# Performance work log

Measured on AMD Instinct MI355X. Metric: run time of the kernel, lower is better.

The kernel has to match this reference:

```python
import jax, jax.numpy as jnp
import numpy as np

N, D = 1024, 64
C = 1.0
MIN_NORM = 1e-15
PROJ_EPS = 4e-3  # HGCN float32 boundary eps


def _artanh(z):
    return jnp.arctanh(jnp.clip(z, -1.0 + 1e-7, 1.0 - 1e-7))


def _mobius_add(x, y, c):
    x2 = jnp.sum(x * x, -1, keepdims=True)
    y2 = jnp.sum(y * y, -1, keepdims=True)
    xy = jnp.sum(x * y, -1, keepdims=True)
    num = (1.0 + 2.0 * c * xy + c * y2) * x + (1.0 - c * x2) * y
    den = 1.0 + 2.0 * c * xy + c * c * x2 * y2
    return num / jnp.maximum(den, MIN_NORM)


def _lambda_x(p, c):
    return 2.0 / jnp.maximum(1.0 - c * jnp.sum(p * p, -1, keepdims=True), MIN_NORM)


def _logmap0(p, c):
    sqrt_c = c ** 0.5
    pn = jnp.maximum(jnp.linalg.norm(p, axis=-1, keepdims=True), MIN_NORM)
    return _artanh(sqrt_c * pn) * p / (sqrt_c * pn)


def _logmap(p1, p2, c):
    # tangent at p1 pointing toward p2 (broadcasts)
    sub = _mobius_add(-p1, p2, c)
    sn = jnp.maximum(jnp.linalg.norm(sub, axis=-1, keepdims=True), MIN_NORM)
    lam = _lambda_x(p1, c)
    sqrt_c = c ** 0.5
    return (2.0 / (sqrt_c * lam)) * _artanh(sqrt_c * sn) * sub / sn


def _expmap(u, p, c):
    # exp at p of tangent u (HGCN signature expmap(u, p, c))
    sqrt_c = c ** 0.5
    un = jnp.maximum(jnp.linalg.norm(u, axis=-1, keepdims=True), MIN_NORM)
    second = jnp.tanh(sqrt_c * _lambda_x(p, c) * un / 2.0) * u / (sqrt_c * un)
    return _mobius_add(p, second, c)


def _proj(x, c):
    sqrt_c = c ** 0.5
    n = jnp.maximum(jnp.linalg.norm(x, axis=-1, keepdims=True), MIN_NORM)
    maxnorm = (1.0 - PROJ_EPS) / sqrt_c
    return jnp.where(n > maxnorm, x / n * maxnorm, x)


def setup_inputs() -> dict:
    key = jax.random.key(0)
    k1, k2, k3 = jax.random.split(key, 3)
    x = 0.1 * jax.random.normal(k1, (N, D), jnp.float32)
    x = _proj(x, C)  # points on the Poincare ball
    adj = (jax.random.uniform(k2, (N, N)) < 0.02).astype(jnp.float32)
    att_W = jax.random.normal(k3, (2 * D, 1), jnp.float32) / np.sqrt(2 * D).astype(np.float32)
    att_b = jnp.zeros((1,), jnp.float32)
    return {"x": x, "adj": adj, "att_W": att_W, "att_b": att_b}


def reference(x, adj, att_W, att_b):
    # x_tangent = logmap0(x)
    x_tan = _logmap0(x, C)
    # DenseAtt: sigmoid(Linear(cat(x_i, x_j))) * adj, without materializing [N,N,2D]
    left = x_tan @ att_W[:D] + att_b   # [N,1]
    right = x_tan @ att_W[D:]          # [N,1]
    adj_att = jax.nn.sigmoid(left + right.T) * adj  # [N,N]
    # local tangent vectors: logmap at x_i of every x_j -> [N,N,D]
    x_local = _logmap(x[:, None, :], x[None, :, :], C)
    support_t = jnp.einsum('ij,ijd->id', adj_att, x_local)  # [N,D]
    return _proj(_expmap(x, support_t, C), C)
```

## Files before the change

kernel.cpp:

```cpp
#include <hip/hip_runtime.h>
#include <math.h>

#define NN 1024
#define DD 64
#define MIN_NORM 1e-15f
#define ART_BOUND (1.0f - 1e-7f)

__device__ __forceinline__ float wave_sum(float v) {
#pragma unroll
    for (int off = 32; off >= 1; off >>= 1)
        v += __shfl_xor(v, off, 64);
    return v;
}

__device__ __forceinline__ float artanh_f(float z) {
    z = fminf(z, ART_BOUND);
    return 0.5f * __logf((1.0f + z) / (1.0f - z));
}

__global__ __launch_bounds__(64) void hypagg_pre_kernel(
    const float* __restrict__ x, const float* __restrict__ W,
    const float* __restrict__ b, float* __restrict__ x2_out,
    float* __restrict__ left_out, float* __restrict__ right_out) {
    const int i = blockIdx.x;
    const int d = threadIdx.x;
    const float xd = x[i * DD + d];
    const float x2 = wave_sum(xd * xd);
    const float pn = fmaxf(sqrtf(x2), MIN_NORM);
    const float xt = artanh_f(pn) * xd / pn;
    const float l = wave_sum(xt * W[d]);
    const float r = wave_sum(xt * W[DD + d]);
    if (d == 0) {
        x2_out[i] = x2;
        left_out[i] = l + b[0];
        right_out[i] = r;
    }
}

__global__ __launch_bounds__(256) void hypagg_main_kernel(
    const float* __restrict__ x, const float* __restrict__ adj,
    const float* __restrict__ x2v, const float* __restrict__ leftv,
    const float* __restrict__ rightv, float* __restrict__ out) {
    __shared__ float sSd[4][DD];
    __shared__ float sAl[4];

    const int i = blockIdx.x;
    const int tid = threadIdx.x;
    const int w = tid >> 6;
    const int lane = tid & 63;

    const float xi = x[i * DD + lane];
    const float x2i = x2v[i];
    const float li = leftv[i];
    const float Bc = 1.0f - x2i;
    const float fac_i = fmaxf(Bc, MIN_NORM);

    float av[4];
#pragma unroll
    for (int kk = 0; kk < 4; ++kk)
        av[kk] = adj[i * NN + (4 * w + kk) * 64 + lane];

    float Sd = 0.0f;
    float alpha = 0.0f;

#pragma unroll
    for (int kk = 0; kk < 4; ++kk) {
        unsigned long long mask = __ballot(av[kk] != 0.0f);
        while (mask) {
            const int bit = __builtin_ctzll(mask);
            mask &= mask - 1;
            const int j = (4 * w + kk) * 64 + bit;
            const float adjv = __shfl(av[kk], bit, 64);
            const float xj = x[j * DD + lane];
            const float y2 = x2v[j];
            const float rj = rightv[j];
            const float dot = wave_sum(xi * xj);
            const float wgt = adjv / (1.0f + __expf(-(li + rj)));
            const float A = 1.0f - 2.0f * dot + y2;
            const float den = fmaxf(1.0f - 2.0f * dot + x2i * y2, MIN_NORM);
            const float sn2 = (A * A * x2i - 2.0f * A * Bc * dot + Bc * Bc * y2) / (den * den);
            const float sn = sqrtf(fmaxf(sn2, 0.0f));
            const float snc = fmaxf(sn, MIN_NORM);
            const float g = wgt * fac_i * artanh_f(sn) / (snc * den);
            Sd += g * xj;
            alpha -= g * A;
        }
    }

    sSd[w][lane] = Sd;
    if (lane == 0) sAl[w] = alpha;
    __syncthreads();

    if (w == 0) {
        const float S = sSd[0][lane] + sSd[1][lane] + sSd[2][lane] + sSd[3][lane];
        const float al = sAl[0] + sAl[1] + sAl[2] + sAl[3];
        const float accd = al * xi + Bc * S;

        const float p2 = wave_sum(accd * accd);
        const float un = fmaxf(sqrtf(x2i), MIN_NORM);
        const float lam_p = 2.0f / fmaxf(1.0f - p2, MIN_NORM);
        const float tt = tanhf(lam_p * un * 0.5f);
        const float second = tt * xi / un;
        const float y2e = wave_sum(second * second);
        const float xye = wave_sum(accd * second);
        const float Ae = 1.0f + 2.0f * xye + y2e;
        const float dene = fmaxf(1.0f + 2.0f * xye + p2 * y2e, MIN_NORM);
        const float res = (Ae * accd + (1.0f - p2) * second) / dene;
        const float n2 = wave_sum(res * res);
        const float n = fmaxf(sqrtf(n2), MIN_NORM);
        const float maxnorm = 1.0f - 4e-3f;
        const float o = (n > maxnorm) ? res * (maxnorm / n) : res;
        out[i * DD + lane] = o;
    }
}

extern "C" void kernel_launch(void* const* d_in, const int* in_sizes, int n_in,
                              void* d_out, int out_size, void* d_ws, size_t ws_size,
                              hipStream_t stream) {
    const float* x   = (const float*)d_in[0];
    const float* adj = (const float*)d_in[1];
    const float* W   = (const float*)d_in[2];
    const float* b   = (const float*)d_in[3];
    float* out = (float*)d_out;

    float* x2v    = (float*)d_ws;
    float* leftv  = x2v + NN;
    float* rightv = leftv + NN;

    hipLaunchKernelGGL(hypagg_pre_kernel, dim3(NN), dim3(DD), 0, stream,
                       x, W, b, x2v, leftv, rightv);
    hipLaunchKernelGGL(hypagg_main_kernel, dim3(NN), dim3(256), 0, stream,
                       x, adj, x2v, leftv, rightv, out);
}
```

Before: 73.94 us.

## Compact neighbor lists in LDS and process neighbor pairs with interleaved reductions

Each wave now compacts its nonzero adjacency entries into a shared-memory list using ballot and mbcnt prefix counts. It then processes neighbors two at a time, so two independent gathers and two shuffle reductions are interleaved and latency can overlap. The pre-kernel packs four rows per 256-thread block to cut block count. The cost is extra LDS, more registers and a tail loop for odd counts.

```diff
diff --git a/kernel.cpp b/kernel.cpp
--- a/kernel.cpp
+++ b/kernel.cpp
@@ -18,12 +18,12 @@
     return 0.5f * __logf((1.0f + z) / (1.0f - z));
 }
 
-__global__ __launch_bounds__(64) void hypagg_pre_kernel(
+__global__ __launch_bounds__(256) void hypagg_pre_kernel(
     const float* __restrict__ x, const float* __restrict__ W,
     const float* __restrict__ b, float* __restrict__ x2_out,
     float* __restrict__ left_out, float* __restrict__ right_out) {
-    const int i = blockIdx.x;
-    const int d = threadIdx.x;
+    const int i = blockIdx.x * 4 + (threadIdx.x >> 6);
+    const int d = threadIdx.x & 63;
     const float xd = x[i * DD + d];
     const float x2 = wave_sum(xd * xd);
     const float pn = fmaxf(sqrtf(x2), MIN_NORM);
@@ -41,6 +41,8 @@
     const float* __restrict__ x, const float* __restrict__ adj,
     const float* __restrict__ x2v, const float* __restrict__ leftv,
     const float* __restrict__ rightv, float* __restrict__ out) {
+    __shared__ int   sjL[4][256];
+    __shared__ float saL[4][256];
     __shared__ float sSd[4][DD];
     __shared__ float sAl[4];
 
@@ -52,29 +54,53 @@
     const float xi = x[i * DD + lane];
     const float x2i = x2v[i];
     const float li = leftv[i];
-    const float Bc = 1.0f - x2i;
-    const float fac_i = fmaxf(Bc, MIN_NORM);
-
     float av[4];
 #pragma unroll
     for (int kk = 0; kk < 4; ++kk)
         av[kk] = adj[i * NN + (4 * w + kk) * 64 + lane];
 
+    const float Bc = 1.0f - x2i;
+    const float fac_i = fmaxf(Bc, MIN_NORM);
+
+    int base = 0;
+#pragma unroll
+    for (int kk = 0; kk < 4; ++kk) {
+        const unsigned long long m = __ballot(av[kk] != 0.0f);
+        if (av[kk] != 0.0f) {
+            const int pos = __builtin_amdgcn_mbcnt_hi(
+                (unsigned int)(m >> 32),
+                __builtin_amdgcn_mbcnt_lo((unsigned int)m, 0u));
+            sjL[w][base + pos] = (4 * w + kk) * 64 + lane;
+            saL[w][base + pos] = av[kk];
+        }
+        base += __popcll(m);
+    }
+    const int M = base;
+
     float Sd = 0.0f;
     float alpha = 0.0f;
 
+    int t = 0;
+    for (; t + 2 <= M; t += 2) {
+        const int ja = sjL[w][t], jb = sjL[w][t + 1];
+        const float aa = saL[w][t], ab = saL[w][t + 1];
+        const float xa = x[ja * DD + lane];
+        const float xb = x[jb * DD + lane];
+        const float y2a = x2v[ja], y2b = x2v[jb];
+        const float rja = rightv[ja], rjb = rightv[jb];
+        float da = xi * xa, db = xi * xb;
 #pragma unroll
-    for (int kk = 0; kk < 4; ++kk) {
-        unsigned long long mask = __ballot(av[kk] != 0.0f);
-        while (mask) {
-            const int bit = __builtin_ctzll(mask);
-            mask &= mask - 1;
-            const int j = (4 * w + kk) * 64 + bit;
-            const float adjv = __shfl(av[kk], bit, 64);
-            const float xj = x[j * DD + lane];
-            const float y2 = x2v[j];
-            const float rj = rightv[j];
-            const float dot = wave_sum(xi * xj);
+        for (int off = 32; off >= 1; off >>= 1) {
+            da += __shfl_xor(da, off, 64);
+            db += __shfl_xor(db, off, 64);
+        }
+#pragma unroll
+        for (int q = 0; q < 2; ++q) {
+            const float dot = (q == 0) ? da : db;
+            const float y2 = (q == 0) ? y2a : y2b;
+            const float rj = (q == 0) ? rja : rjb;
+            const float adjv = (q == 0) ? aa : ab;
+            const float xq = (q == 0) ? xa : xb;
             const float wgt = adjv / (1.0f + __expf(-(li + rj)));
             const float A = 1.0f - 2.0f * dot + y2;
             const float den = fmaxf(1.0f - 2.0f * dot + x2i * y2, MIN_NORM);
@@ -82,9 +108,26 @@
             const float sn = sqrtf(fmaxf(sn2, 0.0f));
             const float snc = fmaxf(sn, MIN_NORM);
             const float g = wgt * fac_i * artanh_f(sn) / (snc * den);
-            Sd += g * xj;
+            Sd += g * xq;
             alpha -= g * A;
         }
+    }
+    for (; t < M; ++t) {
+        const int j = sjL[w][t];
+        const float adjv = saL[w][t];
+        const float xj = x[j * DD + lane];
+        const float y2 = x2v[j];
+        const float rj = rightv[j];
+        const float dot = wave_sum(xi * xj);
+        const float wgt = adjv / (1.0f + __expf(-(li + rj)));
+        const float A = 1.0f - 2.0f * dot + y2;
+        const float den = fmaxf(1.0f - 2.0f * dot + x2i * y2, MIN_NORM);
+        const float sn2 = (A * A * x2i - 2.0f * A * Bc * dot + Bc * Bc * y2) / (den * den);
+        const float sn = sqrtf(fmaxf(sn2, 0.0f));
+        const float snc = fmaxf(sn, MIN_NORM);
+        const float g = wgt * fac_i * artanh_f(sn) / (snc * den);
+        Sd += g * xj;
+        alpha -= g * A;
     }
 
     sSd[w][lane] = Sd;
@@ -127,7 +170,7 @@
     float* leftv  = x2v + NN;
     float* rightv = leftv + NN;
 
-    hipLaunchKernelGGL(hypagg_pre_kernel, dim3(NN), dim3(DD), 0, stream,
+    hipLaunchKernelGGL(hypagg_pre_kernel, dim3(NN / 4), dim3(256), 0, stream,
                        x, W, b, x2v, leftv, rightv);
     hipLaunchKernelGGL(hypagg_main_kernel, dim3(NN), dim3(256), 0, stream,
                        x, adj, x2v, leftv, rightv, out);
```

New measurement: 73.22 us. About the same (-1.0%).
